# Performance work log

Hardware: AMD Instinct MI355X
Metric: run time of the kernel (lower is better)

The kernel has to match this reference:

```python
import jax, jax.numpy as jnp
import numpy as np

N, E, F_NODE, F_EDGE, H, L, G = 4096, 12288, 64, 16, 128, 4, 256
BN_EPS = 1e-5


def setup_inputs() -> dict:
    key = jax.random.key(0)
    ks = jax.random.split(key, 20)
    s = lambda k, shape, fan: jax.random.normal(k, shape, jnp.float32) * (1.0 / np.sqrt(fan))
    inp = {
        'x': jax.random.normal(ks[0], (N, F_NODE), jnp.float32),
        'edge_index': jax.random.randint(ks[1], (2, E), 0, N, dtype=jnp.int64),
        'edge_attr': jax.random.normal(ks[2], (E, F_EDGE), jnp.float32),
        'batch': jnp.sort(jax.random.randint(ks[3], (N,), 0, G, dtype=jnp.int64)),
        # node encoder
        'node_w': s(ks[4], (F_NODE, H), F_NODE),
        'node_b': jnp.zeros((H,), jnp.float32),
        # per-layer edge MLP: edge_feat -> 128 -> H*H
        'e1_w': s(ks[5], (L, F_EDGE, 128), F_EDGE),
        'e1_b': jnp.zeros((L, 128), jnp.float32),
        'e2_w': s(ks[6], (L, 128, H * H), 128) * 0.1,
        'e2_b': jnp.zeros((L, H * H), jnp.float32),
        # NNConv root weight + bias
        'root_w': s(ks[7], (L, H, H), H),
        'conv_b': jnp.zeros((L, H), jnp.float32),
        # batchnorm affine
        'bn_g': jnp.ones((L, H), jnp.float32),
        'bn_b': jnp.zeros((L, H), jnp.float32),
        # head
        'head_w1': s(ks[8], (H, H), H),
        'head_b1': jnp.zeros((H,), jnp.float32),
        'head_w2': s(ks[9], (H, 1), H),
        'head_b2': jnp.zeros((1,), jnp.float32),
    }
    return inp


def reference(x, edge_index, edge_attr, batch, node_w, node_b, e1_w, e1_b,
              e2_w, e2_b, root_w, conv_b, bn_g, bn_b, head_w1, head_b1,
              head_w2, head_b2):
    src, dst = edge_index[0], edge_index[1]
    h = x @ node_w + node_b  # [N,H]
    # in-degree for mean aggregation
    deg = jax.ops.segment_sum(jnp.ones((E,), h.dtype), dst, num_segments=N)
    inv_deg = jnp.where(deg > 0, 1.0 / jnp.maximum(deg, 1.0), 0.0)[:, None]
    for l in range(L):
        # edge MLP -> per-edge [H,H] weight
        e = jax.nn.relu(edge_attr @ e1_w[l] + e1_b[l])            # [E,128]
        W_e = (e @ e2_w[l] + e2_b[l]).reshape(E, H, H)            # [E,H,H]
        msg = jnp.einsum('eh,eho->eo', h[src], W_e)               # [E,H]
        agg = jax.ops.segment_sum(msg, dst, num_segments=N) * inv_deg
        out = agg + h @ root_w[l] + conv_b[l]
        # batchnorm (training-mode batch stats, biased var as in torch)
        mu = out.mean(0)
        var = out.var(0)
        out = (out - mu) * jax.lax.rsqrt(var + BN_EPS) * bn_g[l] + bn_b[l]
        h = h + jax.nn.relu(out)  # dropout disabled (eval)
    # global mean pool over graphs
    cnt = jax.ops.segment_sum(jnp.ones((N,), h.dtype), batch, num_segments=G)
    pooled = jax.ops.segment_sum(h, batch, num_segments=G) / jnp.maximum(cnt, 1.0)[:, None]
    y = jax.nn.relu(pooled @ head_w1 + head_b1) @ head_w2 + head_b2
    return y.squeeze(-1)  # [G]
```

## Files before the change

kernel.cpp:

```cpp
#include <hip/hip_runtime.h>

#define N_NODES 4096
#define E_TOT   12288
#define F_NODE  64
#define F_EDGE  16
#define HDIM    128
#define NLAYER  4
#define NGRAPH  256

typedef _Float16 half8 __attribute__((ext_vector_type(8)));
typedef float    f32x4 __attribute__((ext_vector_type(4)));

__global__ void k_prep_w2(const float* __restrict__ e2w, const float* __restrict__ e2b,
                          _Float16* __restrict__ W2F)
{
    int t = blockIdx.x * 256 + threadIdx.x;
    const int PER_L = 129 * 16384;
    if (t >= NLAYER * PER_L) return;
    int l   = t / PER_L;
    int r   = t - l * PER_L;
    int k   = r >> 14;
    int rem = r & 16383;
    int chunk = rem >> 9;
    int lane  = (rem >> 3) & 63;
    int j     = rem & 7;
    int hc = chunk >> 3, ot = chunk & 7;
    int h  = hc * 32 + (lane >> 4) * 8 + j;
    int o  = ot * 16 + (lane & 15);
    float v;
    if (k < 128) v = e2w[((size_t)(l * 128 + k)) * 16384 + h * 128 + o];
    else         v = e2b[(size_t)l * 16384 + h * 128 + o];
    W2F[t] = (_Float16)v;
}

__global__ __launch_bounds__(128)
void k_node_enc(const float* __restrict__ x, const float* __restrict__ nw,
                const float* __restrict__ nb, float* __restrict__ h,
                _Float16* __restrict__ hf)
{
    __shared__ float xl[F_NODE];
    int n = blockIdx.x, o = threadIdx.x;
    if (o < F_NODE) xl[o] = x[(size_t)n * F_NODE + o];
    __syncthreads();
    float acc = nb[o];
#pragma unroll 8
    for (int f = 0; f < F_NODE; ++f) acc += xl[f] * nw[f * HDIM + o];
    h [(size_t)n * HDIM + o] = acc;
    hf[(size_t)n * HDIM + o] = (_Float16)acc;
}

__global__ void k_deg(const int* __restrict__ dst, int* __restrict__ deg)
{
    int e = blockIdx.x * 256 + threadIdx.x;
    if (e < E_TOT) atomicAdd(&deg[dst[e]], 1);
}

__global__ void k_invd(const int* __restrict__ deg, float* __restrict__ invd)
{
    int n = blockIdx.x * 256 + threadIdx.x;
    if (n < N_NODES) invd[n] = deg[n] > 0 ? 1.0f / (float)deg[n] : 0.0f;
}

#define EF_STRIDE 136
__global__ __launch_bounds__(256)
void k_edge_mlp(const float* __restrict__ ea, const float* __restrict__ w1,
                const float* __restrict__ b1, _Float16* __restrict__ efg)
{
    __shared__ float al[16][17];
    __shared__ float wl[16][HDIM];
    __shared__ float bl[HDIM];
    int t = threadIdx.x, e0 = blockIdx.x * 16;
    if (t < HDIM) bl[t] = b1[t];
    for (int i = t; i < F_EDGE * HDIM; i += 256) wl[i >> 7][i & 127] = w1[i];
    { int i = t; al[i >> 4][i & 15] = ea[(size_t)e0 * F_EDGE + i]; }
    __syncthreads();
    int e = t >> 4, og = t & 15;
    float acc[8];
#pragma unroll
    for (int j = 0; j < 8; ++j) acc[j] = bl[og * 8 + j];
#pragma unroll
    for (int f = 0; f < F_EDGE; ++f) {
        float a = al[e][f];
#pragma unroll
        for (int j = 0; j < 8; ++j) acc[j] += a * wl[f][og * 8 + j];
    }
    half8 o;
#pragma unroll
    for (int j = 0; j < 8; ++j) o[j] = (_Float16)fmaxf(acc[j], 0.f);
    *(half8*)&efg[(size_t)(e0 + e) * EF_STRIDE + og * 8] = o;
    if (og == 0) efg[(size_t)(e0 + e) * EF_STRIDE + 128] = (_Float16)1.0f;
}

#define BM 64
__global__ __launch_bounds__(256, 3)
void k_msg(const _Float16* __restrict__ W2L,
           const _Float16* __restrict__ efg,
           const _Float16* __restrict__ hf,
           const int* __restrict__ srcIdx,
           const int* __restrict__ dstIdx,
           float* __restrict__ agg,
           float* __restrict__ bns1,
           float* __restrict__ bns2)
{
    __shared__ _Float16 efs[BM][40];

    const int tid  = threadIdx.x;
    const int lane = tid & 63;
    const int w    = tid >> 6;
    const int lhi  = lane >> 4;
    const int llo  = lane & 15;

    const int bx    = blockIdx.x;
    const int ks    = (bx & 7) >> 1;
    const int tile  = (bx >> 3) * 2 + (bx & 1);
    const int e0    = tile * BM;
    const int kbase = (129 * ks) >> 2;
    const int kcnt  = ((129 * (ks + 1)) >> 2) - kbase;

    if (bx == 0) {
        if (tid < HDIM)            bns1[tid] = 0.f;
        else if (tid < 2 * HDIM)   bns2[tid - HDIM] = 0.f;
    }

    for (int i = tid; i < BM * 5; i += 256) {
        int r = i / 5, c = i - r * 5;
        *(half8*)&efs[r][c * 8] =
            *(const half8*)(efg + (size_t)(e0 + r) * EF_STRIDE + kbase + c * 8);
    }

    half8 hs[4][4];
#pragma unroll
    for (int rf = 0; rf < 4; ++rf) {
        int s = srcIdx[e0 + rf * 16 + llo];
        const _Float16* hp = hf + (size_t)s * HDIM + lhi * 8;
#pragma unroll
        for (int hc = 0; hc < 4; ++hc)
            hs[rf][hc] = *(const half8*)(hp + hc * 32);
    }

    __syncthreads();

    const _Float16* bp = W2L + (size_t)kbase * 16384 + (w * 2) * 512 + lane * 8;

#define LDQ(d0, d1, kk, hc) do {                                            \
        const _Float16* p_ = bp + (size_t)(kk) * 16384 + (hc) * 4096;       \
        d0 = *(const half8*)(p_); d1 = *(const half8*)(p_ + 512);           \
    } while (0)

    half8 b00, b01, b10, b11, b20, b21, b30, b31;
    LDQ(b00, b01, 0, 0);
    LDQ(b10, b11, 0, 1);
    LDQ(b20, b21, 0, 2);
    LDQ(b30, b31, 0, 3);

    f32x4 acc[4][2];
#pragma unroll
    for (int rf = 0; rf < 4; ++rf)
#pragma unroll
        for (int cf = 0; cf < 2; ++cf)
#pragma unroll
            for (int d = 0; d < 4; ++d) acc[rf][cf][d] = 0.f;

    _Float16 efc[4];
#pragma unroll
    for (int rf = 0; rf < 4; ++rf) efc[rf] = efs[rf * 16 + llo][0];

    for (int kk = 0; kk < kcnt; ++kk) {
        const bool nx = (kk + 1 < kcnt);
        _Float16 efn[4];
        const int kn = nx ? kk + 1 : kk;
#pragma unroll
        for (int rf = 0; rf < 4; ++rf) efn[rf] = efs[rf * 16 + llo][kn];

#pragma unroll
        for (int rf = 0; rf < 4; ++rf) {
            half8 av = hs[rf][0] * efc[rf];
            acc[rf][0] = __builtin_amdgcn_mfma_f32_16x16x32_f16(av, b00, acc[rf][0], 0, 0, 0);
            acc[rf][1] = __builtin_amdgcn_mfma_f32_16x16x32_f16(av, b01, acc[rf][1], 0, 0, 0);
        }
        if (nx) LDQ(b00, b01, kk + 1, 0);

#pragma unroll
        for (int rf = 0; rf < 4; ++rf) {
            half8 av = hs[rf][1] * efc[rf];
            acc[rf][0] = __builtin_amdgcn_mfma_f32_16x16x32_f16(av, b10, acc[rf][0], 0, 0, 0);
            acc[rf][1] = __builtin_amdgcn_mfma_f32_16x16x32_f16(av, b11, acc[rf][1], 0, 0, 0);
        }
        if (nx) LDQ(b10, b11, kk + 1, 1);

#pragma unroll
        for (int rf = 0; rf < 4; ++rf) {
            half8 av = hs[rf][2] * efc[rf];
            acc[rf][0] = __builtin_amdgcn_mfma_f32_16x16x32_f16(av, b20, acc[rf][0], 0, 0, 0);
            acc[rf][1] = __builtin_amdgcn_mfma_f32_16x16x32_f16(av, b21, acc[rf][1], 0, 0, 0);
        }
        if (nx) LDQ(b20, b21, kk + 1, 2);

#pragma unroll
        for (int rf = 0; rf < 4; ++rf) {
            half8 av = hs[rf][3] * efc[rf];
            acc[rf][0] = __builtin_amdgcn_mfma_f32_16x16x32_f16(av, b30, acc[rf][0], 0, 0, 0);
            acc[rf][1] = __builtin_amdgcn_mfma_f32_16x16x32_f16(av, b31, acc[rf][1], 0, 0, 0);
        }
        if (nx) LDQ(b30, b31, kk + 1, 3);

#pragma unroll
        for (int rf = 0; rf < 4; ++rf) efc[rf] = efn[rf];
    }
#undef LDQ

#pragma unroll
    for (int rf = 0; rf < 4; ++rf) {
#pragma unroll
        for (int r = 0; r < 4; ++r) {
            int row = rf * 16 + lhi * 4 + r;
            int d   = dstIdx[e0 + row];
#pragma unroll
            for (int cf = 0; cf < 2; ++cf) {
                int o = w * 32 + cf * 16 + llo;
                atomicAdd(&agg[(size_t)d * HDIM + o], acc[rf][cf][r]);
            }
        }
    }
}

__global__ __launch_bounds__(128)
void k_out(const float* __restrict__ agg, const float* __restrict__ invd,
           const float* __restrict__ h, const float* __restrict__ rw,
           const float* __restrict__ cb, float* __restrict__ outb,
           float* __restrict__ bns1, float* __restrict__ bns2)
{
    __shared__ float hl[16][HDIM];
    int n0 = blockIdx.x * 16, o = threadIdx.x;
    for (int r = 0; r < 16; ++r) hl[r][o] = h[(size_t)(n0 + r) * HDIM + o];
    __syncthreads();
    float acc[16];
    float cbv = cb[o];
#pragma unroll
    for (int r = 0; r < 16; ++r)
        acc[r] = agg[(size_t)(n0 + r) * HDIM + o] * invd[n0 + r] + cbv;
    for (int hh = 0; hh < HDIM; ++hh) {
        float wv = rw[hh * HDIM + o];
#pragma unroll
        for (int r = 0; r < 16; ++r) acc[r] += hl[r][hh] * wv;
    }
    float s1 = 0.f, s2 = 0.f;
#pragma unroll
    for (int r = 0; r < 16; ++r) {
        outb[(size_t)(n0 + r) * HDIM + o] = acc[r];
        s1 += acc[r];
        s2 += acc[r] * acc[r];
    }
    atomicAdd(&bns1[o], s1);
    atomicAdd(&bns2[o], s2);
}

__global__ void k_bn_apply(const float* __restrict__ outb, const float* __restrict__ bns1,
                           const float* __restrict__ bns2, const float* __restrict__ g,
                           const float* __restrict__ b, float* __restrict__ h,
                           _Float16* __restrict__ hf, float* __restrict__ agg,
                           const int* __restrict__ batch, float* __restrict__ pooled,
                           int* __restrict__ cnt, int last)
{
    int i = blockIdx.x * 256 + threadIdx.x;
    int o = i & (HDIM - 1);
    const float inv_n = 1.0f / (float)N_NODES;
    float m   = bns1[o] * inv_n;
    float var = bns2[o] * inv_n - m * m;
    float rs  = rsqrtf(var + 1e-5f);
    float v  = (outb[i] - m) * rs * g[o] + b[o];
    float hn = h[i] + fmaxf(v, 0.f);
    h[i]  = hn;
    hf[i] = (_Float16)hn;
    if (!last) {
        agg[i] = 0.f;
    } else {
        int n  = i >> 7;
        int gg = batch[n];
        atomicAdd(&pooled[(size_t)gg * HDIM + o], hn);
        if (o == 0) atomicAdd(&cnt[gg], 1);
    }
}

__global__ __launch_bounds__(128)
void k_head(const float* __restrict__ pooled, const int* __restrict__ cnt,
            const float* __restrict__ w1, const float* __restrict__ b1,
            const float* __restrict__ w2, const float* __restrict__ b2,
            float* __restrict__ y)
{
    __shared__ float pl[HDIM];
    __shared__ float red[HDIM];
    int g = blockIdx.x, o = threadIdx.x;
    float ic = 1.0f / (float)max(cnt[g], 1);
    pl[o] = pooled[(size_t)g * HDIM + o] * ic;
    __syncthreads();
    float t = b1[o];
#pragma unroll 8
    for (int hh = 0; hh < HDIM; ++hh) t += pl[hh] * w1[hh * HDIM + o];
    t = fmaxf(t, 0.f);
    red[o] = t * w2[o];
    __syncthreads();
    for (int s = 64; s > 0; s >>= 1) {
        if (o < s) red[o] += red[o + s];
        __syncthreads();
    }
    if (o == 0) y[g] = red[0] + b2[0];
}

extern "C" void kernel_launch(void* const* d_in, const int* in_sizes, int n_in,
                              void* d_out, int out_size, void* d_ws, size_t ws_size,
                              hipStream_t stream)
{
    const float* x      = (const float*)d_in[0];
    const int*   ei     = (const int*)  d_in[1];
    const float* ea     = (const float*)d_in[2];
    const int*   batch  = (const int*)  d_in[3];
    const float* node_w = (const float*)d_in[4];
    const float* node_b = (const float*)d_in[5];
    const float* e1w    = (const float*)d_in[6];
    const float* e1b    = (const float*)d_in[7];
    const float* e2w    = (const float*)d_in[8];
    const float* e2b    = (const float*)d_in[9];
    const float* rw     = (const float*)d_in[10];
    const float* cb     = (const float*)d_in[11];
    const float* bng    = (const float*)d_in[12];
    const float* bnb    = (const float*)d_in[13];
    const float* hw1    = (const float*)d_in[14];
    const float* hb1    = (const float*)d_in[15];
    const float* hw2    = (const float*)d_in[16];
    const float* hb2    = (const float*)d_in[17];
    float* y = (float*)d_out;

    char* ws = (char*)d_ws;
    _Float16* W2F  = (_Float16*)ws; ws += 16908288;
    float*    h    = (float*)ws;    ws += 2097152;
    _Float16* hf   = (_Float16*)ws; ws += 1048576;
    _Float16* efg  = (_Float16*)ws; ws += 3342336;
    float*    agg  = (float*)ws;    ws += 2097152;
    float*    bns1 = (float*)ws;    ws += 512;
    float*    bns2 = (float*)ws;    ws += 512;
    float*    outb = (float*)ws;    ws += 2097152;
    int*      deg  = (int*)ws;      ws += 16384;
    float*    invd = (float*)ws;    ws += 16384;
    float*    pooled = (float*)ws;  ws += 131072;
    int*      cnt  = (int*)ws;      ws += 1024;

    const int* src = ei;
    const int* dst = ei + E_TOT;

    k_prep_w2<<<33024, 256, 0, stream>>>(e2w, e2b, W2F);
    k_node_enc<<<N_NODES, 128, 0, stream>>>(x, node_w, node_b, h, hf);
    hipMemsetAsync(deg, 0, N_NODES * sizeof(int), stream);
    k_deg<<<(E_TOT + 255) / 256, 256, 0, stream>>>(dst, deg);
    k_invd<<<(N_NODES + 255) / 256, 256, 0, stream>>>(deg, invd);
    hipMemsetAsync(agg, 0, (size_t)N_NODES * HDIM * sizeof(float), stream);
    hipMemsetAsync(pooled, 0, (size_t)NGRAPH * HDIM * sizeof(float) + NGRAPH * sizeof(int), stream);

    for (int l = 0; l < NLAYER; ++l) {
        k_edge_mlp<<<E_TOT / 16, 256, 0, stream>>>(ea, e1w + l * F_EDGE * HDIM,
                                                   e1b + l * HDIM, efg);
        k_msg<<<(E_TOT / BM) * 4, 256, 0, stream>>>(W2F + (size_t)l * 129 * 16384,
                                                    efg, hf, src, dst, agg, bns1, bns2);
        k_out<<<N_NODES / 16, 128, 0, stream>>>(agg, invd, h,
                                                rw + l * HDIM * HDIM,
                                                cb + l * HDIM, outb, bns1, bns2);
        k_bn_apply<<<(N_NODES * HDIM) / 256, 256, 0, stream>>>(
            outb, bns1, bns2, bng + l * HDIM, bnb + l * HDIM, h, hf,
            agg, batch, pooled, cnt, (l == NLAYER - 1) ? 1 : 0);
    }

    k_head<<<NGRAPH, 128, 0, stream>>>(pooled, cnt, hw1, hb1, hw2, hb2, y);
}
```

Measured before the change: 416.5 us.

## Coalesce W2 prep via LDS transpose and split message k-loop eight ways

k_prep_w2 now has one block per (layer, k) slice. Each block reads e2w with coalesced float4 loads, scatters into an LDS tile in the MFMA fragment layout, and writes the tile out with half8 stores, replacing the old strided gather. k_msg splits the 129-long k dimension into 8 pieces instead of 4, which doubles the grid and asks for 4 waves per SIMD. It also drops the efs prefetch of the next k value. The cost is twice as many float atomicAdds into agg, and less latency hiding on each block's shorter k loop.

```diff
diff --git a/kernel.cpp b/kernel.cpp
--- a/kernel.cpp
+++ b/kernel.cpp
@@ -10,27 +10,39 @@
 
 typedef _Float16 half8 __attribute__((ext_vector_type(8)));
 typedef float    f32x4 __attribute__((ext_vector_type(4)));
-
-__global__ void k_prep_w2(const float* __restrict__ e2w, const float* __restrict__ e2b,
-                          _Float16* __restrict__ W2F)
-{
-    int t = blockIdx.x * 256 + threadIdx.x;
-    const int PER_L = 129 * 16384;
-    if (t >= NLAYER * PER_L) return;
-    int l   = t / PER_L;
-    int r   = t - l * PER_L;
-    int k   = r >> 14;
-    int rem = r & 16383;
-    int chunk = rem >> 9;
-    int lane  = (rem >> 3) & 63;
-    int j     = rem & 7;
-    int hc = chunk >> 3, ot = chunk & 7;
-    int h  = hc * 32 + (lane >> 4) * 8 + j;
-    int o  = ot * 16 + (lane & 15);
-    float v;
-    if (k < 128) v = e2w[((size_t)(l * 128 + k)) * 16384 + h * 128 + o];
-    else         v = e2b[(size_t)l * 16384 + h * 128 + o];
-    W2F[t] = (_Float16)v;
+typedef float    f32x4v __attribute__((ext_vector_type(4)));
+
+__global__ __launch_bounds__(256)
+void k_prep_w2(const float* __restrict__ e2w, const float* __restrict__ e2b,
+               _Float16* __restrict__ W2F)
+{
+    __shared__ _Float16 pg[16384];
+    int b = blockIdx.x;
+    int l = b / 129, k = b - l * 129;
+    const float* src = (k < 128) ? (e2w + ((size_t)(l * 128 + k)) * 16384)
+                                 : (e2b + (size_t)l * 16384);
+    int t = threadIdx.x;
+#pragma unroll
+    for (int it = 0; it < 16; ++it) {
+        int p = it * 1024 + t * 4;
+        float4 v = *(const float4*)(src + p);
+#pragma unroll
+        for (int j4 = 0; j4 < 4; ++j4) {
+            int p_ = p + j4;
+            int h  = p_ >> 7, o = p_ & 127;
+            int idx = ((h >> 5) * 8 + (o >> 4)) * 512
+                    + (((h >> 3) & 3) * 16 + (o & 15)) * 8 + (h & 7);
+            float val = (j4 == 0) ? v.x : (j4 == 1) ? v.y : (j4 == 2) ? v.z : v.w;
+            pg[idx] = (_Float16)val;
+        }
+    }
+    __syncthreads();
+    _Float16* dst = W2F + (size_t)b * 16384;
+#pragma unroll
+    for (int it = 0; it < 8; ++it) {
+        int i = it * 2048 + t * 8;
+        *(half8*)(dst + i) = *(const half8*)(pg + i);
+    }
 }
 
 __global__ __launch_bounds__(128)
@@ -92,7 +104,8 @@
 }
 
 #define BM 64
-__global__ __launch_bounds__(256, 3)
+#define KSPLIT 8
+__global__ __launch_bounds__(256, 4)
 void k_msg(const _Float16* __restrict__ W2L,
            const _Float16* __restrict__ efg,
            const _Float16* __restrict__ hf,
@@ -102,7 +115,7 @@
            float* __restrict__ bns1,
            float* __restrict__ bns2)
 {
-    __shared__ _Float16 efs[BM][40];
+    __shared__ _Float16 efs[BM][24];
 
     const int tid  = threadIdx.x;
     const int lane = tid & 63;
@@ -111,19 +124,19 @@
     const int llo  = lane & 15;
 
     const int bx    = blockIdx.x;
-    const int ks    = (bx & 7) >> 1;
-    const int tile  = (bx >> 3) * 2 + (bx & 1);
+    const int ks    = bx & 7;
+    const int tile  = bx >> 3;
     const int e0    = tile * BM;
-    const int kbase = (129 * ks) >> 2;
-    const int kcnt  = ((129 * (ks + 1)) >> 2) - kbase;
+    const int kbase = (129 * ks) >> 3;
+    const int kcnt  = ((129 * (ks + 1)) >> 3) - kbase;
 
     if (bx == 0) {
         if (tid < HDIM)            bns1[tid] = 0.f;
         else if (tid < 2 * HDIM)   bns2[tid - HDIM] = 0.f;
     }
 
-    for (int i = tid; i < BM * 5; i += 256) {
-        int r = i / 5, c = i - r * 5;
+    if (tid < BM * 3) {
+        int r = tid / 3, c = tid - r * 3;
         *(half8*)&efs[r][c * 8] =
             *(const half8*)(efg + (size_t)(e0 + r) * EF_STRIDE + kbase + c * 8);
     }
@@ -137,6 +150,8 @@
         for (int hc = 0; hc < 4; ++hc)
             hs[rf][hc] = *(const half8*)(hp + hc * 32);
     }
+
+    asm volatile("s_waitcnt vmcnt(0) lgkmcnt(0)" ::: "memory");
 
     __syncthreads();
 
@@ -161,20 +176,15 @@
 #pragma unroll
             for (int d = 0; d < 4; ++d) acc[rf][cf][d] = 0.f;
 
-    _Float16 efc[4];
-#pragma unroll
-    for (int rf = 0; rf < 4; ++rf) efc[rf] = efs[rf * 16 + llo][0];
-
     for (int kk = 0; kk < kcnt; ++kk) {
         const bool nx = (kk + 1 < kcnt);
-        _Float16 efn[4];
-        const int kn = nx ? kk + 1 : kk;
-#pragma unroll
-        for (int rf = 0; rf < 4; ++rf) efn[rf] = efs[rf * 16 + llo][kn];
+        _Float16 efv[4];
+#pragma unroll
+        for (int rf = 0; rf < 4; ++rf) efv[rf] = efs[rf * 16 + llo][kk];
 
 #pragma unroll
         for (int rf = 0; rf < 4; ++rf) {
-            half8 av = hs[rf][0] * efc[rf];
+            half8 av = hs[rf][0] * efv[rf];
             acc[rf][0] = __builtin_amdgcn_mfma_f32_16x16x32_f16(av, b00, acc[rf][0], 0, 0, 0);
             acc[rf][1] = __builtin_amdgcn_mfma_f32_16x16x32_f16(av, b01, acc[rf][1], 0, 0, 0);
         }
@@ -182,7 +192,7 @@
 
 #pragma unroll
         for (int rf = 0; rf < 4; ++rf) {
-            half8 av = hs[rf][1] * efc[rf];
+            half8 av = hs[rf][1] * efv[rf];
             acc[rf][0] = __builtin_amdgcn_mfma_f32_16x16x32_f16(av, b10, acc[rf][0], 0, 0, 0);
             acc[rf][1] = __builtin_amdgcn_mfma_f32_16x16x32_f16(av, b11, acc[rf][1], 0, 0, 0);
         }
@@ -190,7 +200,7 @@
 
 #pragma unroll
         for (int rf = 0; rf < 4; ++rf) {
-            half8 av = hs[rf][2] * efc[rf];
+            half8 av = hs[rf][2] * efv[rf];
             acc[rf][0] = __builtin_amdgcn_mfma_f32_16x16x32_f16(av, b20, acc[rf][0], 0, 0, 0);
             acc[rf][1] = __builtin_amdgcn_mfma_f32_16x16x32_f16(av, b21, acc[rf][1], 0, 0, 0);
         }
@@ -198,14 +208,11 @@
 
 #pragma unroll
         for (int rf = 0; rf < 4; ++rf) {
-            half8 av = hs[rf][3] * efc[rf];
+            half8 av = hs[rf][3] * efv[rf];
             acc[rf][0] = __builtin_amdgcn_mfma_f32_16x16x32_f16(av, b30, acc[rf][0], 0, 0, 0);
             acc[rf][1] = __builtin_amdgcn_mfma_f32_16x16x32_f16(av, b31, acc[rf][1], 0, 0, 0);
         }
         if (nx) LDQ(b30, b31, kk + 1, 3);
-
-#pragma unroll
-        for (int rf = 0; rf < 4; ++rf) efc[rf] = efn[rf];
     }
 #undef LDQ
 
@@ -348,7 +355,7 @@
     const int* src = ei;
     const int* dst = ei + E_TOT;
 
-    k_prep_w2<<<33024, 256, 0, stream>>>(e2w, e2b, W2F);
+    k_prep_w2<<<NLAYER * 129, 256, 0, stream>>>(e2w, e2b, W2F);
     k_node_enc<<<N_NODES, 128, 0, stream>>>(x, node_w, node_b, h, hf);
     hipMemsetAsync(deg, 0, N_NODES * sizeof(int), stream);
     k_deg<<<(E_TOT + 255) / 256, 256, 0, stream>>>(dst, deg);
@@ -359,8 +366,8 @@
     for (int l = 0; l < NLAYER; ++l) {
         k_edge_mlp<<<E_TOT / 16, 256, 0, stream>>>(ea, e1w + l * F_EDGE * HDIM,
                                                    e1b + l * HDIM, efg);
-        k_msg<<<(E_TOT / BM) * 4, 256, 0, stream>>>(W2F + (size_t)l * 129 * 16384,
-                                                    efg, hf, src, dst, agg, bns1, bns2);
+        k_msg<<<(E_TOT / BM) * KSPLIT, 256, 0, stream>>>(
+            W2F + (size_t)l * 129 * 16384, efg, hf, src, dst, agg, bns1, bns2);
         k_out<<<N_NODES / 16, 128, 0, stream>>>(agg, invd, h,
                                                 rw + l * HDIM * HDIM,
                                                 cb + l * HDIM, outb, bns1, bns2);
```

Measured after the change: 636.0 us. 52.7% more time.
